# Performance work log

Measured on AMD Instinct MI355X. Metric: run time of the kernel, lower is better.

The kernel has to match this reference:

```python
import jax, jax.numpy as jnp
import numpy as np

B, S, D, H = 2, 2048, 1024, 16
DK = D // H

def setup_inputs() -> dict:
    key = jax.random.key(0)
    k1, k2, k3 = jax.random.split(key, 3)
    std = 2.0 / (D + 3 * D)
    x = jax.random.normal(k1, (B, S, D), dtype=jnp.float32)
    W_qkv = jax.random.normal(k2, (3 * D, D), dtype=jnp.float32) * std
    W_out = jax.random.normal(k3, (D, D), dtype=jnp.float32) * (2.0 / (2 * D))
    return {"x": x, "W_qkv": W_qkv, "W_out": W_out}

def reference(x, W_qkv, W_out):
    # fused QKV projection: [..., d_in] x [d_out, d_in] -> [..., d_out]
    proj = jnp.einsum('bsd,ed->bse', x, W_qkv)               # [B,S,3*H*DK]
    proj = proj.reshape(B, S, 3, H, DK)
    q = proj[:, :, 0].transpose(0, 2, 1, 3)                  # [B,H,S,DK]
    k = proj[:, :, 1].transpose(0, 2, 1, 3)
    v = proj[:, :, 2].transpose(0, 2, 1, 3)
    scores = jnp.einsum('bhnd,bhmd->bhnm', q, k) / jnp.sqrt(jnp.float32(DK))
    causal = jnp.tril(jnp.ones((S, S), dtype=bool))
    scores = jnp.where(causal, scores, -jnp.inf)
    attn = jax.nn.softmax(scores, axis=-1)
    out = jnp.einsum('bhnm,bhmd->bhnd', attn, v)             # [B,H,S,DK]
    out = out.transpose(0, 2, 1, 3).reshape(B, S, H * DK)
    return jnp.einsum('bsd,ed->bse', out, W_out)             # [B,S,D]
```

## Files before the change

kernel.cpp:

```cpp
#include <hip/hip_runtime.h>
#include <hip/hip_bf16.h>
#include <stdint.h>

typedef __attribute__((ext_vector_type(8))) __bf16 bf16x8;
typedef __attribute__((ext_vector_type(8))) short  short8;
typedef __attribute__((ext_vector_type(4))) float  f32x4;

#define MFMA16(a, b, c) __builtin_amdgcn_mfma_f32_16x16x32_bf16((a), (b), (c), 0, 0, 0)

__device__ __forceinline__ unsigned short f32_bf16(float f) {
  union { float f; unsigned u; } v; v.f = f;
  unsigned r = v.u + 0x7FFFu + ((v.u >> 16) & 1u);
  return (unsigned short)(r >> 16);
}

__device__ __forceinline__ void gload16(const unsigned short* g, unsigned short* l) {
  __builtin_amdgcn_global_load_lds(
      (const __attribute__((address_space(1))) unsigned int*)(g),
      (__attribute__((address_space(3))) unsigned int*)(l), 16, 0, 0);
}

__global__ void cvt3_kernel(const float* __restrict__ a, int na4,
                            const float* __restrict__ b, int nb4,
                            const float* __restrict__ c, int nc4,
                            unsigned short* __restrict__ oa,
                            unsigned short* __restrict__ ob,
                            unsigned short* __restrict__ oc) {
  int total = na4 + nb4 + nc4;
  for (int i = blockIdx.x * blockDim.x + threadIdx.x; i < total; i += gridDim.x * blockDim.x) {
    const float* src; unsigned short* dst; int j = i;
    if (j < na4) { src = a; dst = oa; }
    else if (j - na4 < nb4) { j -= na4; src = b; dst = ob; }
    else { j -= na4 + nb4; src = c; dst = oc; }
    float4 v = reinterpret_cast<const float4*>(src)[j];
    ushort4 o4;
    o4.x = f32_bf16(v.x); o4.y = f32_bf16(v.y);
    o4.z = f32_bf16(v.z); o4.w = f32_bf16(v.w);
    reinterpret_cast<ushort4*>(dst)[j] = o4;
  }
}

__global__ __launch_bounds__(512, 2) void gemm_qkv_8ph(const unsigned short* __restrict__ A,
                                                       const unsigned short* __restrict__ Bm,
                                                       unsigned short* __restrict__ qkv) {
  extern __shared__ unsigned short SM[];
  const int tid  = threadIdx.x;
  const int lane = tid & 63;
  const int w    = tid >> 6;
  const int wr   = w >> 2, wc = w & 3;
  const int l16  = lane & 15, lh = lane >> 4;
  const int sw   = l16 & 7;
  const int m0   = blockIdx.y * 256;
  const int n0   = blockIdx.x * 256;

  f32x4 acc[8][4];
#pragma unroll
  for (int mi = 0; mi < 8; ++mi)
#pragma unroll
    for (int ni = 0; ni < 4; ++ni) acc[mi][ni] = 0.f;

  const int r0 = tid >> 3,         h0 = (tid & 7) ^ (r0 & 7);
  const int r1 = (tid + 512) >> 3, h1 = (tid & 7) ^ (r1 & 7);
  const unsigned short* Asrc[2][2];
  const unsigned short* Bsrc[2][2];
  Asrc[0][0] = A + (size_t)(m0 + r0) * 1024 + h0 * 8;
  Asrc[0][1] = A + (size_t)(m0 + r1) * 1024 + h1 * 8;
  Asrc[1][0] = A + (size_t)(m0 + 128 + r0) * 1024 + h0 * 8;
  Asrc[1][1] = A + (size_t)(m0 + 128 + r1) * 1024 + h1 * 8;
  Bsrc[0][0] = Bm + (size_t)(n0 + r0) * 1024 + h0 * 8;
  Bsrc[0][1] = Bm + (size_t)(n0 + r1) * 1024 + h1 * 8;
  Bsrc[1][0] = Bm + (size_t)(n0 + 128 + r0) * 1024 + h0 * 8;
  Bsrc[1][1] = Bm + (size_t)(n0 + 128 + r1) * 1024 + h1 * 8;
  const int ld0 = (w * 64) * 8;
  const int ld1 = (512 + w * 64) * 8;

#define STAGE_A(buf, h, U) do { \
    gload16(Asrc[h][0] + (U) * 64, SM + (buf) * 32768 + (h) * 8192 + ld0); \
    gload16(Asrc[h][1] + (U) * 64, SM + (buf) * 32768 + (h) * 8192 + ld1); } while (0)
#define STAGE_B(buf, h, U) do { \
    gload16(Bsrc[h][0] + (U) * 64, SM + (buf) * 32768 + 16384 + (h) * 8192 + ld0); \
    gload16(Bsrc[h][1] + (U) * 64, SM + (buf) * 32768 + 16384 + (h) * 8192 + ld1); } while (0)

  STAGE_A(0, 0, 0); STAGE_A(0, 1, 0);
  STAGE_B(0, 0, 0); STAGE_B(0, 1, 0);
  STAGE_B(1, 0, 1); STAGE_B(1, 1, 1);
  asm volatile("s_waitcnt vmcnt(4)" ::: "memory");
  __builtin_amdgcn_s_barrier();

  const int NT = 16;
#pragma unroll 2
  for (int U = 0; U < NT; ++U) {
    const int b = U & 1;
    const unsigned short* Ab = SM + b * 32768 + wr * 8192;
    const unsigned short* Bb = SM + b * 32768 + 16384 + (wc >> 1) * 8192;
    const int rB = (wc & 1) * 64;
    bf16x8 bfr[4][2], af[2][2];

#define LDA(i, j) (*(const bf16x8*)(Ab + (((i) * 16 + l16) * 8 + (((j) * 4 + lh) ^ sw)) * 8))
#define LDB(n, j) (*(const bf16x8*)(Bb + (((rB + (n) * 16 + l16)) * 8 + (((j) * 4 + lh) ^ sw)) * 8))
#define PHASE_MFMA(p) \
    __builtin_amdgcn_s_setprio(1); \
    _Pragma("unroll") \
    for (int n = 0; n < 4; ++n) { \
      acc[2*(p)][n]   = MFMA16(af[0][0], bfr[n][0], acc[2*(p)][n]); \
      acc[2*(p)][n]   = MFMA16(af[0][1], bfr[n][1], acc[2*(p)][n]); \
      acc[2*(p)+1][n] = MFMA16(af[1][0], bfr[n][0], acc[2*(p)+1][n]); \
      acc[2*(p)+1][n] = MFMA16(af[1][1], bfr[n][1], acc[2*(p)+1][n]); \
    } \
    __builtin_amdgcn_s_setprio(0);

    af[0][0] = LDA(0, 0); af[0][1] = LDA(0, 1);
    af[1][0] = LDA(1, 0); af[1][1] = LDA(1, 1);
#pragma unroll
    for (int n = 0; n < 4; ++n) { bfr[n][0] = LDB(n, 0); bfr[n][1] = LDB(n, 1); }
    if (U + 1 < NT) STAGE_A(b ^ 1, 0, U + 1);
    __builtin_amdgcn_s_barrier();
    PHASE_MFMA(0)
    __builtin_amdgcn_s_barrier();
    af[0][0] = LDA(2, 0); af[0][1] = LDA(2, 1);
    af[1][0] = LDA(3, 0); af[1][1] = LDA(3, 1);
    if (U + 1 < NT) STAGE_A(b ^ 1, 1, U + 1);
    __builtin_amdgcn_s_barrier();
    PHASE_MFMA(1)
    __builtin_amdgcn_s_barrier();
    af[0][0] = LDA(4, 0); af[0][1] = LDA(4, 1);
    af[1][0] = LDA(5, 0); af[1][1] = LDA(5, 1);
    if (U + 2 < NT) STAGE_B(b, 0, U + 2);
    __builtin_amdgcn_s_barrier();
    PHASE_MFMA(2)
    __builtin_amdgcn_s_barrier();
    af[0][0] = LDA(6, 0); af[0][1] = LDA(6, 1);
    af[1][0] = LDA(7, 0); af[1][1] = LDA(7, 1);
    if (U + 2 < NT) STAGE_B(b, 1, U + 2);
    __builtin_amdgcn_s_barrier();
    PHASE_MFMA(3)
    asm volatile("s_waitcnt vmcnt(4)" ::: "memory");
    __builtin_amdgcn_s_barrier();
#undef LDA
#undef LDB
#undef PHASE_MFMA
  }

  __syncthreads();
  unsigned short* Ep = SM + w * 8192;
  const int gn0 = n0 + wc * 64;
  const int cc  = gn0 >> 10;
  const int hh2 = (gn0 & 1023) >> 6;
  const int gm0 = m0 + wr * 128;
  const int bb2 = gm0 >> 11;
  const int ss0 = gm0 & 2047;
  const int bh2 = bb2 * 16 + hh2;

  if (cc < 2) {
    const float qsc = (cc == 0) ? 0.18033688f : 1.0f;
#pragma unroll
    for (int mi = 0; mi < 8; ++mi)
#pragma unroll
      for (int ni = 0; ni < 4; ++ni)
#pragma unroll
        for (int r = 0; r < 4; ++r) {
          int row = mi * 16 + lh * 4 + r;
          int col = (ni * 16 + l16) ^ (lh << 3);
          Ep[row * 64 + col] = f32_bf16(acc[mi][ni][r] * qsc);
        }
    unsigned short* qk = qkv + (((size_t)cc * 32 + bh2) * 2048 + ss0) * 64;
#pragma unroll
    for (int it = 0; it < 16; ++it) {
      int ci = it * 64 + lane;
      int row = ci >> 3, c = ci & 7;
      short8 vv = *(const short8*)(Ep + row * 64 + ((c ^ ((row >> 2) & 3)) * 8));
      *(short8*)(qk + (size_t)row * 64 + c * 8) = vv;
    }
  } else {
#pragma unroll
    for (int mi = 0; mi < 8; ++mi)
#pragma unroll
      for (int ni = 0; ni < 4; ++ni) {
        int dk = ni * 16 + l16;
        int ssl = mi * 16 + lh * 4;
        unsigned lo, hi;
        asm("v_cvt_pk_bf16_f32 %0, %1, %2" : "=v"(lo) : "v"(acc[mi][ni][0]), "v"(acc[mi][ni][1]));
        asm("v_cvt_pk_bf16_f32 %0, %1, %2" : "=v"(hi) : "v"(acc[mi][ni][2]), "v"(acc[mi][ni][3]));
        int off = dk * 128 + (ssl ^ ((dk & 7) << 3));
        *(uint2*)(Ep + off) = make_uint2(lo, hi);
      }
    unsigned short* vt = qkv + (size_t)8388608 + (size_t)bh2 * 64 * 2048 + ss0;
#pragma unroll
    for (int it = 0; it < 16; ++it) {
      int ci = it * 64 + lane;
      int dk = ci >> 4, c = ci & 15;
      short8 vv = *(const short8*)(Ep + dk * 128 + ((c ^ (dk & 7)) * 8));
      *(short8*)(vt + (size_t)dk * 2048 + c * 8) = vv;
    }
  }
#undef STAGE_A
#undef STAGE_B
}

__global__ __launch_bounds__(256) void gemm_out(const unsigned short* __restrict__ A,
                                                const unsigned short* __restrict__ Bm,
                                                float* __restrict__ C,
                                                int M, int N, int K) {
  extern __shared__ unsigned short SM[];
  unsigned short* As = SM;
  unsigned short* Bs = SM + 4096;
  const int tid  = threadIdx.x;
  const int lane = tid & 63;
  const int wid  = tid >> 6;
  const int wr   = wid >> 1, wc = wid & 1;
  const int l16  = lane & 15, lh = lane >> 4;
  const int m0   = blockIdx.y * 128;
  const int n0   = blockIdx.x * 128;

  f32x4 acc[4][4];
#pragma unroll
  for (int mi = 0; mi < 4; ++mi)
#pragma unroll
    for (int ni = 0; ni < 4; ++ni) acc[mi][ni] = 0.f;

  const int c0 = tid, c1 = 256 + tid;
  const unsigned short* a0 = A + (size_t)(m0 + (c0 >> 2)) * K + (c0 & 3) * 8;
  const unsigned short* a1 = A + (size_t)(m0 + (c1 >> 2)) * K + (c1 & 3) * 8;
  const unsigned short* b0 = Bm + (size_t)(n0 + (c0 >> 2)) * K + (c0 & 3) * 8;
  const unsigned short* b1 = Bm + (size_t)(n0 + (c1 >> 2)) * K + (c1 & 3) * 8;
  const int d0 = wid * 64 * 8;
  const int d1 = (256 + wid * 64) * 8;

  for (int k0 = 0; k0 < K; k0 += 32) {
    __syncthreads();
    gload16(a0 + k0, As + d0);
    gload16(a1 + k0, As + d1);
    gload16(b0 + k0, Bs + d0);
    gload16(b1 + k0, Bs + d1);
    __syncthreads();
    bf16x8 af[4], bfr[4];
#pragma unroll
    for (int i = 0; i < 4; ++i) {
      af[i]  = *(const bf16x8*)(As + (wr * 64 + i * 16 + l16) * 32 + lh * 8);
      bfr[i] = *(const bf16x8*)(Bs + (wc * 64 + i * 16 + l16) * 32 + lh * 8);
    }
#pragma unroll
    for (int mi = 0; mi < 4; ++mi)
#pragma unroll
      for (int ni = 0; ni < 4; ++ni)
        acc[mi][ni] = MFMA16(af[mi], bfr[ni], acc[mi][ni]);
  }

  __syncthreads();
  float* Ef = (float*)(SM + wid * 4096);
  const int gm0 = m0 + wr * 64;
  const int gn0 = n0 + wc * 64;
#pragma unroll
  for (int p = 0; p < 2; ++p) {
#pragma unroll
    for (int mi = 0; mi < 4; ++mi)
#pragma unroll
      for (int q = 0; q < 2; ++q) {
        int ni = 2 * p + q;
#pragma unroll
        for (int r = 0; r < 4; ++r) {
          int row = mi * 16 + lh * 4 + r;
          int col = (q * 16 + l16) ^ ((row & 7) << 2);
          Ef[row * 32 + col] = acc[mi][ni][r];
        }
      }
#pragma unroll
    for (int it = 0; it < 8; ++it) {
      int ci = it * 64 + lane;
      int row = ci >> 3, c4 = ci & 7;
      float4 vv = *(const float4*)(Ef + row * 32 + ((c4 * 4) ^ ((row & 7) << 2)));
      *(float4*)(&C[(size_t)(gm0 + row) * N + gn0 + p * 32 + c4 * 4]) = vv;
    }
  }
}

__global__ __launch_bounds__(256) void attn_kernel(const unsigned short* __restrict__ Qg,
                                                   const unsigned short* __restrict__ Kg,
                                                   const unsigned short* __restrict__ Vtg,
                                                   unsigned short* __restrict__ Og) {
  __shared__ unsigned short Ks[2][64 * 64];
  __shared__ unsigned short Vs[2][64 * 64];
  __shared__ unsigned short Pl[4][16 * 64];

  const int tid  = threadIdx.x;
  const int lane = tid & 63;
  const int w    = tid >> 6;
  const int l16  = lane & 15, lh = lane >> 4;
  const int j    = blockIdx.x >> 5;
  const int ring = j >> 3, k = j & 7;
  const int qt   = (ring == 0) ? 31 - k : (ring == 1) ? k : (ring == 2) ? 23 - k : 8 + k;
  const int bh   = blockIdx.x & 31;
  const int bb   = bh >> 4, hh = bh & 15;
  const int qb   = qt * 64;
  const int wqb  = qb + w * 16;

  const unsigned short* Qh = Qg + (size_t)bh * (2048 * 64);
  const unsigned short* Kh = Kg + (size_t)bh * (2048 * 64);
  const unsigned short* Vh = Vtg + (size_t)bh * (64 * 2048);

  bf16x8 qf[2];
#pragma unroll
  for (int h2 = 0; h2 < 2; ++h2)
    qf[h2] = *(const bf16x8*)(Qh + (size_t)(wqb + l16) * 64 + h2 * 32 + lh * 8);

  float mreg = 0.f;
  float ll   = 0.f;
  f32x4 o[4];
#pragma unroll
  for (int f = 0; f < 4; ++f) o[f] = 0.f;

  const int sA = tid, sB = tid + 256;
  const int rA = sA >> 3, hA = (sA & 7) ^ (rA & 7);
  const int rB = sB >> 3, hB = (sB & 7) ^ (rB & 7);
  const unsigned short* kSrcA = Kh + rA * 64 + hA * 8;
  const unsigned short* kSrcB = Kh + rB * 64 + hB * 8;
  const unsigned short* vSrcA = Vh + (size_t)rA * 2048 + hA * 8;
  const unsigned short* vSrcB = Vh + (size_t)rB * 2048 + hB * 8;
  const int ldsA = w * 64 * 8;
  const int ldsB = (256 + w * 64) * 8;

  const int sw = l16 & 7;
  const int ntiles = qt + 1;

  gload16(kSrcA, &Ks[0][ldsA]);
  gload16(kSrcB, &Ks[0][ldsB]);
  gload16(vSrcA, &Vs[0][ldsA]);
  gload16(vSrcB, &Vs[0][ldsB]);
  __syncthreads();

  for (int t = 0; t < ntiles; ++t) {
    const int kv0 = t * 64;
    const int cur = t & 1;
    if (t + 1 < ntiles) {
      const int nk = kv0 + 64;
      gload16(kSrcA + (size_t)nk * 64, &Ks[cur ^ 1][ldsA]);
      gload16(kSrcB + (size_t)nk * 64, &Ks[cur ^ 1][ldsB]);
      gload16(vSrcA + nk, &Vs[cur ^ 1][ldsA]);
      gload16(vSrcB + nk, &Vs[cur ^ 1][ldsB]);
    }

    {
      const unsigned short* Kb = Ks[cur];
      const unsigned short* Vb = Vs[cur];
      __builtin_amdgcn_s_setprio(1);

      f32x4 st[4];
#pragma unroll
      for (int tt = 0; tt < 4; ++tt) {
        const unsigned short* krow = Kb + (tt * 16 + l16) * 64;
        bf16x8 kf0 = *(const bf16x8*)(krow + ((lh ^ sw) * 8));
        bf16x8 kf1 = *(const bf16x8*)(krow + (((lh + 4) ^ sw) * 8));
        f32x4 a = {0.f, 0.f, 0.f, 0.f};
        a = MFMA16(kf0, qf[0], a);
        a = MFMA16(kf1, qf[1], a);
        st[tt] = a;
      }

      if (kv0 + 63 > wqb) {
        int qrow = wqb + l16;
#pragma unroll
        for (int tt = 0; tt < 4; ++tt) {
          int kvb = kv0 + tt * 16 + lh * 4;
#pragma unroll
          for (int r = 0; r < 4; ++r)
            if (kvb + r > qrow) st[tt][r] = -__builtin_inff();
        }
      }

      float pm = fmaxf(fmaxf(st[0][0], st[0][1]), fmaxf(st[0][2], st[0][3]));
#pragma unroll
      for (int tt = 1; tt < 4; ++tt)
        pm = fmaxf(pm, fmaxf(fmaxf(st[tt][0], st[tt][1]), fmaxf(st[tt][2], st[tt][3])));
      if (!__all(pm <= mreg + 8.f)) {
        float t0 = pm;
        t0 = fmaxf(t0, __shfl_xor(t0, 16));
        t0 = fmaxf(t0, __shfl_xor(t0, 32));
        float mn = fmaxf(mreg, t0);
        float er = exp2f(mreg - mn);
        mreg = mn;
        ll *= er;
#pragma unroll
        for (int r = 0; r < 4; ++r) {
          float e = __shfl(er, lh * 4 + r);
#pragma unroll
          for (int f = 0; f < 4; ++f) o[f][r] *= e;
        }
      }

      unsigned short* Pw = Pl[w];
      int rbase = l16 * 64;
      float ps = 0.f;
#pragma unroll
      for (int tt = 0; tt < 4; ++tt) {
        float p0 = exp2f(st[tt][0] - mreg);
        float p1 = exp2f(st[tt][1] - mreg);
        float p2 = exp2f(st[tt][2] - mreg);
        float p3 = exp2f(st[tt][3] - mreg);
        ps += (p0 + p1) + (p2 + p3);
        unsigned lo, hi;
        asm("v_cvt_pk_bf16_f32 %0, %1, %2" : "=v"(lo) : "v"(p0), "v"(p1));
        asm("v_cvt_pk_bf16_f32 %0, %1, %2" : "=v"(hi) : "v"(p2), "v"(p3));
        int c8 = tt * 2 + (lh >> 1);
        int off = rbase + ((c8 ^ sw) << 3) + (lh & 1) * 4;
        *(uint2*)(Pw + off) = make_uint2(lo, hi);
      }
      float rs = ps;
      rs += __shfl_xor(rs, 16);
      rs += __shfl_xor(rs, 32);
      ll += rs;

      bf16x8 pf0 = *(const bf16x8*)(Pw + rbase + ((lh ^ sw) * 8));
      bf16x8 pf1 = *(const bf16x8*)(Pw + rbase + (((lh + 4) ^ sw) * 8));
#pragma unroll
      for (int f = 0; f < 4; ++f) {
        const unsigned short* vrow = Vb + (f * 16 + l16) * 64;
        bf16x8 vf0 = *(const bf16x8*)(vrow + ((lh ^ sw) * 8));
        bf16x8 vf1 = *(const bf16x8*)(vrow + (((lh + 4) ^ sw) * 8));
        o[f] = MFMA16(pf0, vf0, o[f]);
        o[f] = MFMA16(pf1, vf1, o[f]);
      }
      __builtin_amdgcn_s_setprio(0);
    }
    __syncthreads();
  }

  unsigned short* op = Og + (size_t)bb * 2048 * 1024 + (size_t)hh * 64;
#pragma unroll
  for (int r = 0; r < 4; ++r) {
    float linv = 1.f / __shfl(ll, lh * 4 + r);
    int row = wqb + lh * 4 + r;
#pragma unroll
    for (int f = 0; f < 4; ++f)
      op[(size_t)row * 1024 + f * 16 + l16] = f32_bf16(o[f][r] * linv);
  }
}

extern "C" void kernel_launch(void* const* d_in, const int* in_sizes, int n_in,
                              void* d_out, int out_size, void* d_ws, size_t ws_size,
                              hipStream_t stream) {
  const float* x    = (const float*)d_in[0];
  const float* Wqkv = (const float*)d_in[1];
  const float* Wout = (const float*)d_in[2];
  float* out = (float*)d_out;

  char* ws = (char*)d_ws;
  unsigned short* xb  = (unsigned short*)(ws);
  unsigned short* wqb = (unsigned short*)(ws + (size_t)8 * 1024 * 1024);
  unsigned short* wob = (unsigned short*)(ws + (size_t)14 * 1024 * 1024);
  unsigned short* qkv = (unsigned short*)(ws + (size_t)16 * 1024 * 1024);
  unsigned short* att = (unsigned short*)(ws + (size_t)40 * 1024 * 1024);

  static bool attr_set = false;
  if (!attr_set) {
    hipFuncSetAttribute((const void*)gemm_qkv_8ph,
                        hipFuncAttributeMaxDynamicSharedMemorySize, 131072);
    attr_set = true;
  }

  cvt3_kernel<<<2048, 256, 0, stream>>>(x, 4194304 / 4, Wqkv, 3145728 / 4,
                                        Wout, 1048576 / 4, xb, wqb, wob);

  gemm_qkv_8ph<<<dim3(12, 16), 512, 131072, stream>>>(xb, wqb, qkv);

  const unsigned short* Qp  = qkv;
  const unsigned short* Kp  = qkv + 4194304;
  const unsigned short* Vtp = qkv + 8388608;
  attn_kernel<<<1024, 256, 0, stream>>>(Qp, Kp, Vtp, att);

  gemm_out<<<dim3(8, 32), 256, 32768, stream>>>(att, wob, out, 4096, 1024, 1024);
}
```

Before: 118.0 us.

## Shrink attention tiles to 32 queries and 32 keys with 2-wave blocks

Measured after the change: 131.6 us. 11.6% more time.

```diff
diff --git a/kernel.cpp b/kernel.cpp
--- a/kernel.cpp
+++ b/kernel.cpp
@@ -274,24 +274,25 @@
   }
 }
 
-__global__ __launch_bounds__(256) void attn_kernel(const unsigned short* __restrict__ Qg,
+__global__ __launch_bounds__(128) void attn_kernel(const unsigned short* __restrict__ Qg,
                                                    const unsigned short* __restrict__ Kg,
                                                    const unsigned short* __restrict__ Vtg,
                                                    unsigned short* __restrict__ Og) {
-  __shared__ unsigned short Ks[2][64 * 64];
-  __shared__ unsigned short Vs[2][64 * 64];
-  __shared__ unsigned short Pl[4][16 * 64];
+  __shared__ unsigned short Ks[2][32 * 64];
+  __shared__ unsigned short Vs[2][64 * 32];
+  __shared__ unsigned short Pl[2][16 * 32];
 
   const int tid  = threadIdx.x;
   const int lane = tid & 63;
   const int w    = tid >> 6;
   const int l16  = lane & 15, lh = lane >> 4;
   const int j    = blockIdx.x >> 5;
-  const int ring = j >> 3, k = j & 7;
-  const int qt   = (ring == 0) ? 31 - k : (ring == 1) ? k : (ring == 2) ? 23 - k : 8 + k;
+  const int k2   = j & 7, ring = j >> 3;
+  const int base = (ring >> 1) * 8 + k2;
+  const int qt   = (ring & 1) ? (63 - base) : base;
   const int bh   = blockIdx.x & 31;
   const int bb   = bh >> 4, hh = bh & 15;
-  const int qb   = qt * 64;
+  const int qb   = qt * 32;
   const int wqb  = qb + w * 16;
 
   const unsigned short* Qh = Qg + (size_t)bh * (2048 * 64);
@@ -309,57 +310,74 @@
 #pragma unroll
   for (int f = 0; f < 4; ++f) o[f] = 0.f;
 
-  const int sA = tid, sB = tid + 256;
-  const int rA = sA >> 3, hA = (sA & 7) ^ (rA & 7);
-  const int rB = sB >> 3, hB = (sB & 7) ^ (rB & 7);
-  const unsigned short* kSrcA = Kh + rA * 64 + hA * 8;
-  const unsigned short* kSrcB = Kh + rB * 64 + hB * 8;
-  const unsigned short* vSrcA = Vh + (size_t)rA * 2048 + hA * 8;
-  const unsigned short* vSrcB = Vh + (size_t)rB * 2048 + hB * 8;
-  const int ldsA = w * 64 * 8;
-  const int ldsB = (256 + w * 64) * 8;
-
   const int sw = l16 & 7;
+
+  const int sk0 = tid, sk1 = tid + 128;
+  const int rk0 = sk0 >> 3, hk0 = (sk0 & 7) ^ (rk0 & 7);
+  const int rk1 = sk1 >> 3, hk1 = (sk1 & 7) ^ (rk1 & 7);
+  const unsigned short* kSrc0 = Kh + rk0 * 64 + hk0 * 8;
+  const unsigned short* kSrc1 = Kh + rk1 * 64 + hk1 * 8;
+  const int rv0 = sk0 >> 2, hv0 = (sk0 & 3) ^ ((rv0 + (rv0 >> 2)) & 3);
+  const int rv1 = sk1 >> 2, hv1 = (sk1 & 3) ^ ((rv1 + (rv1 >> 2)) & 3);
+  const unsigned short* vSrc0 = Vh + (size_t)rv0 * 2048 + hv0 * 8;
+  const unsigned short* vSrc1 = Vh + (size_t)rv1 * 2048 + hv1 * 8;
+  const int lds0 = (w * 64) * 8;
+  const int lds1 = (w * 64 + 128) * 8;
+
+  int koff[2][2], voff[4];
+#pragma unroll
+  for (int tt = 0; tt < 2; ++tt) {
+    int krow = tt * 16 + l16;
+    koff[tt][0] = krow * 64 + ((lh ^ sw) << 3);
+    koff[tt][1] = krow * 64 + (((lh + 4) ^ sw) << 3);
+  }
+#pragma unroll
+  for (int f = 0; f < 4; ++f) {
+    int vrow = f * 16 + l16;
+    voff[f] = vrow * 32 + ((lh ^ ((vrow + (vrow >> 2)) & 3)) << 3);
+  }
+  const int pwoff0 = l16 * 32 + (((0 * 4 + lh) ^ (l16 & 6)) << 2);
+  const int pwoff1 = l16 * 32 + (((1 * 4 + lh) ^ (l16 & 6)) << 2);
+  const int proff  = l16 * 32 + (((2 * lh) ^ (l16 & 6)) << 2);
+
   const int ntiles = qt + 1;
 
-  gload16(kSrcA, &Ks[0][ldsA]);
-  gload16(kSrcB, &Ks[0][ldsB]);
-  gload16(vSrcA, &Vs[0][ldsA]);
-  gload16(vSrcB, &Vs[0][ldsB]);
+  gload16(kSrc0, &Ks[0][lds0]);
+  gload16(kSrc1, &Ks[0][lds1]);
+  gload16(vSrc0, &Vs[0][lds0]);
+  gload16(vSrc1, &Vs[0][lds1]);
   __syncthreads();
 
   for (int t = 0; t < ntiles; ++t) {
-    const int kv0 = t * 64;
+    const int kv0 = t * 32;
     const int cur = t & 1;
     if (t + 1 < ntiles) {
-      const int nk = kv0 + 64;
-      gload16(kSrcA + (size_t)nk * 64, &Ks[cur ^ 1][ldsA]);
-      gload16(kSrcB + (size_t)nk * 64, &Ks[cur ^ 1][ldsB]);
-      gload16(vSrcA + nk, &Vs[cur ^ 1][ldsA]);
-      gload16(vSrcB + nk, &Vs[cur ^ 1][ldsB]);
-    }
-
-    {
+      const int nk = kv0 + 32;
+      gload16(kSrc0 + (size_t)nk * 64, &Ks[cur ^ 1][lds0]);
+      gload16(kSrc1 + (size_t)nk * 64, &Ks[cur ^ 1][lds1]);
+      gload16(vSrc0 + nk, &Vs[cur ^ 1][lds0]);
+      gload16(vSrc1 + nk, &Vs[cur ^ 1][lds1]);
+    }
+
+    if (kv0 <= wqb + 15) {
       const unsigned short* Kb = Ks[cur];
       const unsigned short* Vb = Vs[cur];
-      __builtin_amdgcn_s_setprio(1);
-
-      f32x4 st[4];
-#pragma unroll
-      for (int tt = 0; tt < 4; ++tt) {
-        const unsigned short* krow = Kb + (tt * 16 + l16) * 64;
-        bf16x8 kf0 = *(const bf16x8*)(krow + ((lh ^ sw) * 8));
-        bf16x8 kf1 = *(const bf16x8*)(krow + (((lh + 4) ^ sw) * 8));
+
+      f32x4 st[2];
+#pragma unroll
+      for (int tt = 0; tt < 2; ++tt) {
+        bf16x8 kf0 = *(const bf16x8*)(Kb + koff[tt][0]);
+        bf16x8 kf1 = *(const bf16x8*)(Kb + koff[tt][1]);
         f32x4 a = {0.f, 0.f, 0.f, 0.f};
         a = MFMA16(kf0, qf[0], a);
         a = MFMA16(kf1, qf[1], a);
         st[tt] = a;
       }
 
-      if (kv0 + 63 > wqb) {
+      if (kv0 + 31 > wqb) {
         int qrow = wqb + l16;
 #pragma unroll
-        for (int tt = 0; tt < 4; ++tt) {
+        for (int tt = 0; tt < 2; ++tt) {
           int kvb = kv0 + tt * 16 + lh * 4;
 #pragma unroll
           for (int r = 0; r < 4; ++r)
@@ -368,9 +386,7 @@
       }
 
       float pm = fmaxf(fmaxf(st[0][0], st[0][1]), fmaxf(st[0][2], st[0][3]));
-#pragma unroll
-      for (int tt = 1; tt < 4; ++tt)
-        pm = fmaxf(pm, fmaxf(fmaxf(st[tt][0], st[tt][1]), fmaxf(st[tt][2], st[tt][3])));
+      pm = fmaxf(pm, fmaxf(fmaxf(st[1][0], st[1][1]), fmaxf(st[1][2], st[1][3])));
       if (!__all(pm <= mreg + 8.f)) {
         float t0 = pm;
         t0 = fmaxf(t0, __shfl_xor(t0, 16));
@@ -388,38 +404,31 @@
       }
 
       unsigned short* Pw = Pl[w];
-      int rbase = l16 * 64;
-      float ps = 0.f;
-#pragma unroll
-      for (int tt = 0; tt < 4; ++tt) {
-        float p0 = exp2f(st[tt][0] - mreg);
-        float p1 = exp2f(st[tt][1] - mreg);
-        float p2 = exp2f(st[tt][2] - mreg);
-        float p3 = exp2f(st[tt][3] - mreg);
-        ps += (p0 + p1) + (p2 + p3);
-        unsigned lo, hi;
-        asm("v_cvt_pk_bf16_f32 %0, %1, %2" : "=v"(lo) : "v"(p0), "v"(p1));
-        asm("v_cvt_pk_bf16_f32 %0, %1, %2" : "=v"(hi) : "v"(p2), "v"(p3));
-        int c8 = tt * 2 + (lh >> 1);
-        int off = rbase + ((c8 ^ sw) << 3) + (lh & 1) * 4;
-        *(uint2*)(Pw + off) = make_uint2(lo, hi);
-      }
-      float rs = ps;
-      rs += __shfl_xor(rs, 16);
-      rs += __shfl_xor(rs, 32);
-      ll += rs;
-
-      bf16x8 pf0 = *(const bf16x8*)(Pw + rbase + ((lh ^ sw) * 8));
-      bf16x8 pf1 = *(const bf16x8*)(Pw + rbase + (((lh + 4) ^ sw) * 8));
+      float ps;
+      {
+        float p0 = exp2f(st[0][0] - mreg), p1 = exp2f(st[0][1] - mreg);
+        float p2 = exp2f(st[0][2] - mreg), p3 = exp2f(st[0][3] - mreg);
+        float q0 = exp2f(st[1][0] - mreg), q1 = exp2f(st[1][1] - mreg);
+        float q2 = exp2f(st[1][2] - mreg), q3 = exp2f(st[1][3] - mreg);
+        ps = ((p0 + p1) + (p2 + p3)) + ((q0 + q1) + (q2 + q3));
+        unsigned w0, w1, w2, w3;
+        asm("v_cvt_pk_bf16_f32 %0, %1, %2" : "=v"(w0) : "v"(p0), "v"(p1));
+        asm("v_cvt_pk_bf16_f32 %0, %1, %2" : "=v"(w1) : "v"(p2), "v"(p3));
+        asm("v_cvt_pk_bf16_f32 %0, %1, %2" : "=v"(w2) : "v"(q0), "v"(q1));
+        asm("v_cvt_pk_bf16_f32 %0, %1, %2" : "=v"(w3) : "v"(q2), "v"(q3));
+        *(uint2*)(Pw + pwoff0) = make_uint2(w0, w1);
+        *(uint2*)(Pw + pwoff1) = make_uint2(w2, w3);
+      }
+      ps += __shfl_xor(ps, 16);
+      ps += __shfl_xor(ps, 32);
+      ll += ps;
+
+      bf16x8 pf = *(const bf16x8*)(Pw + proff);
 #pragma unroll
       for (int f = 0; f < 4; ++f) {
-        const unsigned short* vrow = Vb + (f * 16 + l16) * 64;
-        bf16x8 vf0 = *(const bf16x8*)(vrow + ((lh ^ sw) * 8));
-        bf16x8 vf1 = *(const bf16x8*)(vrow + (((lh + 4) ^ sw) * 8));
-        o[f] = MFMA16(pf0, vf0, o[f]);
-        o[f] = MFMA16(pf1, vf1, o[f]);
-      }
-      __builtin_amdgcn_s_setprio(0);
+        bf16x8 vf = *(const bf16x8*)(Vb + voff[f]);
+        o[f] = MFMA16(pf, vf, o[f]);
+      }
     }
     __syncthreads();
   }
@@ -465,7 +474,7 @@
   const unsigned short* Qp  = qkv;
   const unsigned short* Kp  = qkv + 4194304;
   const unsigned short* Vtp = qkv + 8388608;
-  attn_kernel<<<1024, 256, 0, stream>>>(Qp, Kp, Vtp, att);
+  attn_kernel<<<2048, 128, 0, stream>>>(Qp, Kp, Vtp, att);
 
   gemm_out<<<dim3(8, 32), 256, 32768, stream>>>(att, wob, out, 4096, 1024, 1024);
 }
```

## Rewrite attention inner loop with 32x32 MFMA and register-resident P

Applied to the files above, without the earlier changes.

Measured after the change: 126.7 us. +7.4%, slower.

```diff
diff --git a/kernel.cpp b/kernel.cpp
--- a/kernel.cpp
+++ b/kernel.cpp
@@ -2,11 +2,13 @@
 #include <hip/hip_bf16.h>
 #include <stdint.h>
 
-typedef __attribute__((ext_vector_type(8))) __bf16 bf16x8;
-typedef __attribute__((ext_vector_type(8))) short  short8;
-typedef __attribute__((ext_vector_type(4))) float  f32x4;
+typedef __attribute__((ext_vector_type(8)))  __bf16 bf16x8;
+typedef __attribute__((ext_vector_type(8)))  short  short8;
+typedef __attribute__((ext_vector_type(4)))  float  f32x4;
+typedef __attribute__((ext_vector_type(16))) float  f32x16;
 
 #define MFMA16(a, b, c) __builtin_amdgcn_mfma_f32_16x16x32_bf16((a), (b), (c), 0, 0, 0)
+#define MFMA32(a, b, c) __builtin_amdgcn_mfma_f32_32x32x16_bf16((a), (b), (c), 0, 0, 0)
 
 __device__ __forceinline__ unsigned short f32_bf16(float f) {
   union { float f; unsigned u; } v; v.f = f;
@@ -274,164 +276,166 @@
   }
 }
 
-__global__ __launch_bounds__(256) void attn_kernel(const unsigned short* __restrict__ Qg,
+__global__ __launch_bounds__(128) void attn_kernel(const unsigned short* __restrict__ Qg,
                                                    const unsigned short* __restrict__ Kg,
                                                    const unsigned short* __restrict__ Vtg,
                                                    unsigned short* __restrict__ Og) {
   __shared__ unsigned short Ks[2][64 * 64];
   __shared__ unsigned short Vs[2][64 * 64];
-  __shared__ unsigned short Pl[4][16 * 64];
 
   const int tid  = threadIdx.x;
   const int lane = tid & 63;
   const int w    = tid >> 6;
-  const int l16  = lane & 15, lh = lane >> 4;
+  const int l31  = lane & 31, hi = lane >> 5;
   const int j    = blockIdx.x >> 5;
   const int ring = j >> 3, k = j & 7;
   const int qt   = (ring == 0) ? 31 - k : (ring == 1) ? k : (ring == 2) ? 23 - k : 8 + k;
   const int bh   = blockIdx.x & 31;
   const int bb   = bh >> 4, hh = bh & 15;
   const int qb   = qt * 64;
-  const int wqb  = qb + w * 16;
+  const int wq   = qb + w * 32;
+  const int qcol = wq + l31;
 
   const unsigned short* Qh = Qg + (size_t)bh * (2048 * 64);
   const unsigned short* Kh = Kg + (size_t)bh * (2048 * 64);
   const unsigned short* Vh = Vtg + (size_t)bh * (64 * 2048);
 
-  bf16x8 qf[2];
-#pragma unroll
-  for (int h2 = 0; h2 < 2; ++h2)
-    qf[h2] = *(const bf16x8*)(Qh + (size_t)(wqb + l16) * 64 + h2 * 32 + lh * 8);
-
-  float mreg = 0.f;
-  float ll   = 0.f;
-  f32x4 o[4];
-#pragma unroll
-  for (int f = 0; f < 4; ++f) o[f] = 0.f;
-
-  const int sA = tid, sB = tid + 256;
-  const int rA = sA >> 3, hA = (sA & 7) ^ (rA & 7);
-  const int rB = sB >> 3, hB = (sB & 7) ^ (rB & 7);
-  const unsigned short* kSrcA = Kh + rA * 64 + hA * 8;
-  const unsigned short* kSrcB = Kh + rB * 64 + hB * 8;
-  const unsigned short* vSrcA = Vh + (size_t)rA * 2048 + hA * 8;
-  const unsigned short* vSrcB = Vh + (size_t)rB * 2048 + hB * 8;
-  const int ldsA = w * 64 * 8;
-  const int ldsB = (256 + w * 64) * 8;
-
-  const int sw = l16 & 7;
-  const int ntiles = qt + 1;
-
-  gload16(kSrcA, &Ks[0][ldsA]);
-  gload16(kSrcB, &Ks[0][ldsB]);
-  gload16(vSrcA, &Vs[0][ldsA]);
-  gload16(vSrcB, &Vs[0][ldsB]);
+  bf16x8 qf[4];
+#pragma unroll
+  for (int ks = 0; ks < 4; ++ks)
+    qf[ks] = *(const bf16x8*)(Qh + (size_t)qcol * 64 + ks * 16 + hi * 8);
+
+  f32x16 o0 = 0.f, o1 = 0.f;
+  float mreg = 0.f, ll = 0.f;
+
+  const unsigned short* kSrc[4];
+  const unsigned short* vSrc[4];
+  int ldso[4];
+#pragma unroll
+  for (int i = 0; i < 4; ++i) {
+    int s = i * 128 + tid;
+    int r = s >> 3, h = (s & 7) ^ (r & 7);
+    kSrc[i] = Kh + r * 64 + h * 8;
+    vSrc[i] = Vh + (size_t)r * 2048 + h * 8;
+    ldso[i] = (i * 128 + w * 64) * 8;
+  }
+
+  const int swz = l31 & 7;
+
+#pragma unroll
+  for (int i = 0; i < 4; ++i) {
+    gload16(kSrc[i], &Ks[0][ldso[i]]);
+    gload16(vSrc[i], &Vs[0][ldso[i]]);
+  }
   __syncthreads();
 
-  for (int t = 0; t < ntiles; ++t) {
+  for (int t = 0; t <= qt; ++t) {
     const int kv0 = t * 64;
     const int cur = t & 1;
-    if (t + 1 < ntiles) {
-      const int nk = kv0 + 64;
-      gload16(kSrcA + (size_t)nk * 64, &Ks[cur ^ 1][ldsA]);
-      gload16(kSrcB + (size_t)nk * 64, &Ks[cur ^ 1][ldsB]);
-      gload16(vSrcA + nk, &Vs[cur ^ 1][ldsA]);
-      gload16(vSrcB + nk, &Vs[cur ^ 1][ldsB]);
-    }
-
-    {
-      const unsigned short* Kb = Ks[cur];
-      const unsigned short* Vb = Vs[cur];
-      __builtin_amdgcn_s_setprio(1);
-
-      f32x4 st[4];
-#pragma unroll
-      for (int tt = 0; tt < 4; ++tt) {
-        const unsigned short* krow = Kb + (tt * 16 + l16) * 64;
-        bf16x8 kf0 = *(const bf16x8*)(krow + ((lh ^ sw) * 8));
-        bf16x8 kf1 = *(const bf16x8*)(krow + (((lh + 4) ^ sw) * 8));
-        f32x4 a = {0.f, 0.f, 0.f, 0.f};
-        a = MFMA16(kf0, qf[0], a);
-        a = MFMA16(kf1, qf[1], a);
-        st[tt] = a;
-      }
-
-      if (kv0 + 63 > wqb) {
-        int qrow = wqb + l16;
-#pragma unroll
-        for (int tt = 0; tt < 4; ++tt) {
-          int kvb = kv0 + tt * 16 + lh * 4;
-#pragma unroll
-          for (int r = 0; r < 4; ++r)
-            if (kvb + r > qrow) st[tt][r] = -__builtin_inff();
-        }
-      }
-
-      float pm = fmaxf(fmaxf(st[0][0], st[0][1]), fmaxf(st[0][2], st[0][3]));
-#pragma unroll
-      for (int tt = 1; tt < 4; ++tt)
-        pm = fmaxf(pm, fmaxf(fmaxf(st[tt][0], st[tt][1]), fmaxf(st[tt][2], st[tt][3])));
-      if (!__all(pm <= mreg + 8.f)) {
-        float t0 = pm;
-        t0 = fmaxf(t0, __shfl_xor(t0, 16));
-        t0 = fmaxf(t0, __shfl_xor(t0, 32));
-        float mn = fmaxf(mreg, t0);
-        float er = exp2f(mreg - mn);
-        mreg = mn;
-        ll *= er;
-#pragma unroll
-        for (int r = 0; r < 4; ++r) {
-          float e = __shfl(er, lh * 4 + r);
-#pragma unroll
-          for (int f = 0; f < 4; ++f) o[f][r] *= e;
-        }
-      }
-
-      unsigned short* Pw = Pl[w];
-      int rbase = l16 * 64;
-      float ps = 0.f;
-#pragma unroll
-      for (int tt = 0; tt < 4; ++tt) {
-        float p0 = exp2f(st[tt][0] - mreg);
-        float p1 = exp2f(st[tt][1] - mreg);
-        float p2 = exp2f(st[tt][2] - mreg);
-        float p3 = exp2f(st[tt][3] - mreg);
-        ps += (p0 + p1) + (p2 + p3);
-        unsigned lo, hi;
-        asm("v_cvt_pk_bf16_f32 %0, %1, %2" : "=v"(lo) : "v"(p0), "v"(p1));
-        asm("v_cvt_pk_bf16_f32 %0, %1, %2" : "=v"(hi) : "v"(p2), "v"(p3));
-        int c8 = tt * 2 + (lh >> 1);
-        int off = rbase + ((c8 ^ sw) << 3) + (lh & 1) * 4;
-        *(uint2*)(Pw + off) = make_uint2(lo, hi);
-      }
-      float rs = ps;
-      rs += __shfl_xor(rs, 16);
-      rs += __shfl_xor(rs, 32);
-      ll += rs;
-
-      bf16x8 pf0 = *(const bf16x8*)(Pw + rbase + ((lh ^ sw) * 8));
-      bf16x8 pf1 = *(const bf16x8*)(Pw + rbase + (((lh + 4) ^ sw) * 8));
-#pragma unroll
-      for (int f = 0; f < 4; ++f) {
-        const unsigned short* vrow = Vb + (f * 16 + l16) * 64;
-        bf16x8 vf0 = *(const bf16x8*)(vrow + ((lh ^ sw) * 8));
-        bf16x8 vf1 = *(const bf16x8*)(vrow + (((lh + 4) ^ sw) * 8));
-        o[f] = MFMA16(pf0, vf0, o[f]);
-        o[f] = MFMA16(pf1, vf1, o[f]);
-      }
-      __builtin_amdgcn_s_setprio(0);
-    }
+    if (t < qt) {
+#pragma unroll
+      for (int i = 0; i < 4; ++i) {
+        gload16(kSrc[i] + (size_t)(kv0 + 64) * 64, &Ks[cur ^ 1][ldso[i]]);
+        gload16(vSrc[i] + (kv0 + 64), &Vs[cur ^ 1][ldso[i]]);
+      }
+    }
+    const unsigned short* Kb = Ks[cur];
+    const unsigned short* Vb = Vs[cur];
+
+    f32x16 s0 = 0.f, s1 = 0.f;
+#pragma unroll
+    for (int ks = 0; ks < 4; ++ks) {
+      int c = (ks * 2 + hi) ^ swz;
+      bf16x8 ka0 = *(const bf16x8*)(Kb + l31 * 64 + c * 8);
+      bf16x8 ka1 = *(const bf16x8*)(Kb + (32 + l31) * 64 + c * 8);
+      s0 = MFMA32(ka0, qf[ks], s0);
+      s1 = MFMA32(ka1, qf[ks], s1);
+    }
+
+    if (t == qt) {
+#pragma unroll
+      for (int r = 0; r < 16; ++r) {
+        int kvp = kv0 + (r & 3) + 8 * (r >> 2) + 4 * hi;
+        if (kvp > qcol)      s0[r] = -__builtin_inff();
+        if (kvp + 32 > qcol) s1[r] = -__builtin_inff();
+      }
+    }
+
+    float pm = fmaxf(s0[0], s1[0]);
+#pragma unroll
+    for (int r = 1; r < 16; ++r) pm = fmaxf(pm, fmaxf(s0[r], s1[r]));
+    if (!__all(pm <= mreg + 8.f)) {
+      float t0 = fmaxf(pm, __shfl_xor(pm, 32));
+      float mn = fmaxf(mreg, t0);
+      float esc = exp2f(mreg - mn);
+      mreg = mn; ll *= esc;
+#pragma unroll
+      for (int r = 0; r < 16; ++r) { o0[r] *= esc; o1[r] *= esc; }
+    }
+
+    float p[32];
+#pragma unroll
+    for (int r = 0; r < 16; ++r) {
+      p[r]      = exp2f(s0[r] - mreg);
+      p[16 + r] = exp2f(s1[r] - mreg);
+    }
+    float ps = p[0];
+#pragma unroll
+    for (int r = 1; r < 32; ++r) ps += p[r];
+    ps += __shfl_xor(ps, 32);
+    ll += ps;
+
+    bf16x8 pf[2][2];
+#pragma unroll
+    for (int kvsub = 0; kvsub < 2; ++kvsub)
+#pragma unroll
+      for (int ks = 0; ks < 2; ++ks) {
+        const int off = kvsub * 16 + ks * 8;
+        unsigned a1, b1, a2, b2;
+        asm("v_cvt_pk_bf16_f32 %0, %1, %2" : "=v"(a1) : "v"(p[off + 0]), "v"(p[off + 1]));
+        asm("v_cvt_pk_bf16_f32 %0, %1, %2" : "=v"(b1) : "v"(p[off + 4]), "v"(p[off + 5]));
+        asm("v_cvt_pk_bf16_f32 %0, %1, %2" : "=v"(a2) : "v"(p[off + 2]), "v"(p[off + 3]));
+        asm("v_cvt_pk_bf16_f32 %0, %1, %2" : "=v"(b2) : "v"(p[off + 6]), "v"(p[off + 7]));
+        asm("v_permlane32_swap_b32 %0, %1" : "+v"(a1), "+v"(b1));
+        asm("v_permlane32_swap_b32 %0, %1" : "+v"(a2), "+v"(b2));
+        union { unsigned u[4]; bf16x8 f; } fr;
+        fr.u[0] = a1; fr.u[1] = a2; fr.u[2] = b1; fr.u[3] = b2;
+        pf[kvsub][ks] = fr.f;
+      }
+
+#pragma unroll
+    for (int kvsub = 0; kvsub < 2; ++kvsub)
+#pragma unroll
+      for (int ks = 0; ks < 2; ++ks) {
+        int c = (kvsub * 4 + ks * 2 + hi) ^ swz;
+        bf16x8 va0 = *(const bf16x8*)(Vb + l31 * 64 + c * 8);
+        bf16x8 va1 = *(const bf16x8*)(Vb + (32 + l31) * 64 + c * 8);
+        o0 = MFMA32(va0, pf[kvsub][ks], o0);
+        o1 = MFMA32(va1, pf[kvsub][ks], o1);
+      }
     __syncthreads();
   }
 
+  unsigned short* slab = &Ks[0][w * 2048];
+  float inv = 1.f / ll;
+#pragma unroll
+  for (int i = 0; i < 8; ++i) {
+    const int r = 2 * i;
+    const int d0 = (r & 3) + 8 * (r >> 2) + 4 * hi;
+    unsigned u0, u1;
+    asm("v_cvt_pk_bf16_f32 %0, %1, %2" : "=v"(u0) : "v"(o0[r] * inv), "v"(o0[r + 1] * inv));
+    asm("v_cvt_pk_bf16_f32 %0, %1, %2" : "=v"(u1) : "v"(o1[r] * inv), "v"(o1[r + 1] * inv));
+    *(unsigned*)(slab + l31 * 64 + (((d0 >> 3) ^ (l31 & 7)) * 8) + (d0 & 7)) = u0;
+    const int d1 = 32 + d0;
+    *(unsigned*)(slab + l31 * 64 + (((d1 >> 3) ^ (l31 & 7)) * 8) + (d1 & 7)) = u1;
+  }
   unsigned short* op = Og + (size_t)bb * 2048 * 1024 + (size_t)hh * 64;
 #pragma unroll
-  for (int r = 0; r < 4; ++r) {
-    float linv = 1.f / __shfl(ll, lh * 4 + r);
-    int row = wqb + lh * 4 + r;
-#pragma unroll
-    for (int f = 0; f < 4; ++f)
-      op[(size_t)row * 1024 + f * 16 + l16] = f32_bf16(o[f][r] * linv);
+  for (int it = 0; it < 4; ++it) {
+    int ci = it * 64 + lane;
+    int qr = ci >> 3, c = ci & 7;
+    short8 vv = *(const short8*)(slab + qr * 64 + ((c ^ (qr & 7)) * 8));
+    *(short8*)(op + (size_t)(wq + qr) * 1024 + c * 8) = vv;
   }
 }
 
@@ -465,7 +469,7 @@
   const unsigned short* Qp  = qkv;
   const unsigned short* Kp  = qkv + 4194304;
   const unsigned short* Vtp = qkv + 8388608;
-  attn_kernel<<<1024, 256, 0, stream>>>(Qp, Kp, Vtp, att);
+  attn_kernel<<<1024, 128, 0, stream>>>(Qp, Kp, Vtp, att);
 
   gemm_out<<<dim3(8, 32), 256, 32768, stream>>>(att, wob, out, 4096, 1024, 1024);
 }
```

## Split long causal attention rows across KV ranges with a merge kernel

Applied to the files above, without the earlier changes.

New measurement: 118.3 us. No clear change (+0.3%).

```diff
diff --git a/kernel.cpp b/kernel.cpp
--- a/kernel.cpp
+++ b/kernel.cpp
@@ -274,10 +274,24 @@
   }
 }
 
+__device__ const signed char JQT[48] = {31,31,30,15, 30,29,29,28,14, 28,27,27,26,13, 26,25,25,24,12,
+                                        24,23,23,22,11, 22,21,21,20,10, 20,19,19,18, 9, 18,17,17,16, 8,
+                                        16, 7, 6, 5, 4, 3, 2, 1, 0};
+__device__ const signed char JS0[48] = { 0,16, 0, 0, 16, 0,15, 0, 0, 15, 0,14, 0, 0, 14, 0,13, 0, 0,
+                                        13, 0,12, 0, 0, 12, 0,11, 0, 0, 11, 0,10, 0, 0, 10, 0, 9, 0, 0,
+                                         9, 0, 0, 0, 0, 0, 0, 0, 0};
+__device__ const signed char JNT[48] = {16,16,16,16, 15,15,15,15,15, 14,14,14,14,14, 13,13,13,13,13,
+                                        12,12,12,12,12, 11,11,11,11,11, 10,10,10,10,10,  9, 9, 9, 9, 9,
+                                         8, 8, 7, 6, 5, 4, 3, 2, 1};
+__device__ const signed char JSL[48] = {30,31,28,-1, 29,26,27,24,-1, 25,22,23,20,-1, 21,18,19,16,-1,
+                                        17,14,15,12,-1, 13,10,11, 8,-1,  9, 6, 7, 4,-1,  5, 2, 3, 0,-1,
+                                         1,-1,-1,-1,-1,-1,-1,-1,-1};
+
 __global__ __launch_bounds__(256) void attn_kernel(const unsigned short* __restrict__ Qg,
                                                    const unsigned short* __restrict__ Kg,
                                                    const unsigned short* __restrict__ Vtg,
-                                                   unsigned short* __restrict__ Og) {
+                                                   unsigned short* __restrict__ Og,
+                                                   char* __restrict__ parts) {
   __shared__ unsigned short Ks[2][64 * 64];
   __shared__ unsigned short Vs[2][64 * 64];
   __shared__ unsigned short Pl[4][16 * 64];
@@ -286,10 +300,14 @@
   const int lane = tid & 63;
   const int w    = tid >> 6;
   const int l16  = lane & 15, lh = lane >> 4;
-  const int j    = blockIdx.x >> 5;
-  const int ring = j >> 3, k = j & 7;
-  const int qt   = (ring == 0) ? 31 - k : (ring == 1) ? k : (ring == 2) ? 23 - k : 8 + k;
+  const int sw   = l16 & 7;
+
+  const int jb   = blockIdx.x >> 5;
   const int bh   = blockIdx.x & 31;
+  const int qt   = JQT[jb];
+  const int ts0  = JS0[jb];
+  const int tend = ts0 + JNT[jb];
+  const int slot = JSL[jb];
   const int bb   = bh >> 4, hh = bh & 15;
   const int qb   = qt * 64;
   const int wqb  = qb + w * 16;
@@ -319,19 +337,16 @@
   const int ldsA = w * 64 * 8;
   const int ldsB = (256 + w * 64) * 8;
 
-  const int sw = l16 & 7;
-  const int ntiles = qt + 1;
-
-  gload16(kSrcA, &Ks[0][ldsA]);
-  gload16(kSrcB, &Ks[0][ldsB]);
-  gload16(vSrcA, &Vs[0][ldsA]);
-  gload16(vSrcB, &Vs[0][ldsB]);
+  gload16(kSrcA + (size_t)(ts0 * 64) * 64, &Ks[0][ldsA]);
+  gload16(kSrcB + (size_t)(ts0 * 64) * 64, &Ks[0][ldsB]);
+  gload16(vSrcA + ts0 * 64, &Vs[0][ldsA]);
+  gload16(vSrcB + ts0 * 64, &Vs[0][ldsB]);
   __syncthreads();
 
-  for (int t = 0; t < ntiles; ++t) {
+  for (int t = ts0; t < tend; ++t) {
     const int kv0 = t * 64;
-    const int cur = t & 1;
-    if (t + 1 < ntiles) {
+    const int cur = (t - ts0) & 1;
+    if (t + 1 < tend) {
       const int nk = kv0 + 64;
       gload16(kSrcA + (size_t)nk * 64, &Ks[cur ^ 1][ldsA]);
       gload16(kSrcB + (size_t)nk * 64, &Ks[cur ^ 1][ldsB]);
@@ -342,7 +357,6 @@
     {
       const unsigned short* Kb = Ks[cur];
       const unsigned short* Vb = Vs[cur];
-      __builtin_amdgcn_s_setprio(1);
 
       f32x4 st[4];
 #pragma unroll
@@ -419,20 +433,90 @@
         o[f] = MFMA16(pf0, vf0, o[f]);
         o[f] = MFMA16(pf1, vf1, o[f]);
       }
-      __builtin_amdgcn_s_setprio(0);
     }
     __syncthreads();
   }
 
-  unsigned short* op = Og + (size_t)bb * 2048 * 1024 + (size_t)hh * 64;
-#pragma unroll
-  for (int r = 0; r < 4; ++r) {
-    float linv = 1.f / __shfl(ll, lh * 4 + r);
-    int row = wqb + lh * 4 + r;
-#pragma unroll
-    for (int f = 0; f < 4; ++f)
-      op[(size_t)row * 1024 + f * 16 + l16] = f32_bf16(o[f][r] * linv);
-  }
+  if (slot < 0) {
+    unsigned short* op = Og + (size_t)bb * 2048 * 1024 + (size_t)hh * 64;
+#pragma unroll
+    for (int r = 0; r < 4; ++r) {
+      float linv = 1.f / __shfl(ll, lh * 4 + r);
+      int row = wqb + lh * 4 + r;
+#pragma unroll
+      for (int f = 0; f < 4; ++f)
+        op[(size_t)row * 1024 + f * 16 + l16] = f32_bf16(o[f][r] * linv);
+    }
+  } else {
+    char* pb = parts + (size_t)(bh * 32 + slot) * 8704;
+    float* pl = (float*)pb;
+    float* pmv = pl + 64;
+    unsigned short* pO = (unsigned short*)(pb + 512);
+    float lv[4], mv[4];
+#pragma unroll
+    for (int r = 0; r < 4; ++r) {
+      lv[r] = __shfl(ll, lh * 4 + r);
+      mv[r] = __shfl(mreg, lh * 4 + r);
+    }
+    if (l16 == 0) {
+#pragma unroll
+      for (int r = 0; r < 4; ++r) {
+        pl[w * 16 + lh * 4 + r]  = lv[r];
+        pmv[w * 16 + lh * 4 + r] = mv[r];
+      }
+    }
+#pragma unroll
+    for (int r = 0; r < 4; ++r)
+#pragma unroll
+      for (int f = 0; f < 4; ++f)
+        pO[(w * 16 + lh * 4 + r) * 64 + f * 16 + l16] = f32_bf16(o[f][r]);
+  }
+}
+
+__global__ __launch_bounds__(256) void merge_kernel(const char* __restrict__ parts,
+                                                    unsigned short* __restrict__ Og) {
+  const int task = blockIdx.x;
+  const int bh = task & 31, qi = task >> 5;
+  const int qt = 16 + qi;
+  const int bb = bh >> 4, hh = bh & 15;
+  const int tid = threadIdx.x;
+  const int r = tid >> 2, q = tid & 3;
+
+  const char* pb1 = parts + (size_t)(bh * 32 + 2 * qi) * 8704;
+  const char* pb2 = parts + (size_t)(bh * 32 + 2 * qi + 1) * 8704;
+  const float* l1p = (const float*)pb1;
+  const float* l2p = (const float*)pb2;
+  float lv1 = l1p[r], mv1 = l1p[64 + r];
+  float lv2 = l2p[r], mv2 = l2p[64 + r];
+  float mx = fmaxf(mv1, mv2);
+  float w1 = exp2f(mv1 - mx), w2 = exp2f(mv2 - mx);
+  float inv = 1.f / (lv1 * w1 + lv2 * w2);
+  float s1 = w1 * inv, s2 = w2 * inv;
+
+  const unsigned short* O1 = (const unsigned short*)(pb1 + 512) + r * 64 + q * 16;
+  const unsigned short* O2 = (const unsigned short*)(pb2 + 512) + r * 64 + q * 16;
+  short8 a0 = *(const short8*)(O1);
+  short8 a1 = *(const short8*)(O1 + 8);
+  short8 b0 = *(const short8*)(O2);
+  short8 b1 = *(const short8*)(O2 + 8);
+
+  unsigned outw[8];
+#pragma unroll
+  for (int i = 0; i < 4; ++i) {
+    float x0 = __builtin_bit_cast(float, ((unsigned)(unsigned short)a0[2 * i]) << 16) * s1 +
+               __builtin_bit_cast(float, ((unsigned)(unsigned short)b0[2 * i]) << 16) * s2;
+    float x1 = __builtin_bit_cast(float, ((unsigned)(unsigned short)a0[2 * i + 1]) << 16) * s1 +
+               __builtin_bit_cast(float, ((unsigned)(unsigned short)b0[2 * i + 1]) << 16) * s2;
+    asm("v_cvt_pk_bf16_f32 %0, %1, %2" : "=v"(outw[i]) : "v"(x0), "v"(x1));
+    float y0 = __builtin_bit_cast(float, ((unsigned)(unsigned short)a1[2 * i]) << 16) * s1 +
+               __builtin_bit_cast(float, ((unsigned)(unsigned short)b1[2 * i]) << 16) * s2;
+    float y1 = __builtin_bit_cast(float, ((unsigned)(unsigned short)a1[2 * i + 1]) << 16) * s1 +
+               __builtin_bit_cast(float, ((unsigned)(unsigned short)b1[2 * i + 1]) << 16) * s2;
+    asm("v_cvt_pk_bf16_f32 %0, %1, %2" : "=v"(outw[4 + i]) : "v"(y0), "v"(y1));
+  }
+  unsigned short* op = Og + ((size_t)bb * 2048 + qt * 64 + r) * 1024 + hh * 64 + q * 16;
+  *(uint4*)(op)     = make_uint4(outw[0], outw[1], outw[2], outw[3]);
+  *(uint4*)(op + 8) = make_uint4(outw[4], outw[5], outw[6], outw[7]);
 }
 
 extern "C" void kernel_launch(void* const* d_in, const int* in_sizes, int n_in,
@@ -449,6 +533,7 @@
   unsigned short* wob = (unsigned short*)(ws + (size_t)14 * 1024 * 1024);
   unsigned short* qkv = (unsigned short*)(ws + (size_t)16 * 1024 * 1024);
   unsigned short* att = (unsigned short*)(ws + (size_t)40 * 1024 * 1024);
+  char* parts = ws;
 
   static bool attr_set = false;
   if (!attr_set) {
@@ -465,7 +550,8 @@
   const unsigned short* Qp  = qkv;
   const unsigned short* Kp  = qkv + 4194304;
   const unsigned short* Vtp = qkv + 8388608;
-  attn_kernel<<<1024, 256, 0, stream>>>(Qp, Kp, Vtp, att);
+  attn_kernel<<<1536, 256, 0, stream>>>(Qp, Kp, Vtp, att, parts);
+  merge_kernel<<<512, 256, 0, stream>>>(parts, att);
 
   gemm_out<<<dim3(8, 32), 256, 32768, stream>>>(att, wob, out, 4096, 1024, 1024);
 }
```
